# Kernel optimization log

Hardware: AMD Instinct MI355X
Metric: run time of the kernel (lower is better)

The kernel has to match this reference:

```python
import jax, jax.numpy as jnp
import numpy as np

B_SZ, SEQ, H, P, N, LBLK = 16, 2048, 16, 64, 16, 64  # batch, seqlen, heads, d_head, d_state, block_len


def setup_inputs() -> dict:
    key = jax.random.key(0)
    k1, k2, k3, k4 = jax.random.split(key, 4)
    X = jax.random.normal(k1, (B_SZ, SEQ, H, P), jnp.float32)
    # A is a per-step log-decay; real Mamba2 has A < 0 so exp(segsum) stays bounded
    A = -0.1 * jax.random.uniform(k2, (B_SZ, SEQ, H), jnp.float32)
    B = jax.random.normal(k3, (B_SZ, SEQ, H, N), jnp.float32)
    C = jax.random.normal(k4, (B_SZ, SEQ, H, N), jnp.float32)
    return {"X": X, "A": A, "B": B, "C": C}


def _exp_segsum(x):
    """x: (..., t). Returns exp(cumsum[i]-cumsum[j]) for j<=i, 0 above diagonal."""
    t = x.shape[-1]
    cs = jnp.cumsum(x, axis=-1)
    diff = cs[..., :, None] - cs[..., None, :]
    mask = jnp.tril(jnp.ones((t, t), dtype=bool))
    return jnp.where(mask, jnp.exp(jnp.where(mask, diff, 0.0)), 0.0)


def ssd_forward(X, A, B, C):
    b, s, h, p = X.shape
    n = B.shape[-1]
    c = s // LBLK
    # chunk: (b, c, l, h, *)
    Xb = X.reshape(b, c, LBLK, h, p)
    Bb = B.reshape(b, c, LBLK, h, n)
    Cb = C.reshape(b, c, LBLK, h, n)
    Ab = jnp.transpose(A.reshape(b, c, LBLK, h), (0, 3, 1, 2))  # (b, h, c, l)
    A_cs = jnp.cumsum(Ab, axis=-1)                               # (b, h, c, l)

    # 1. intra-chunk (diagonal block) output: kernel 1
    L = _exp_segsum(Ab)                                          # (b, h, c, l, s)
    CB = jnp.einsum("bclhn,bcshn->bhcls", Cb, Bb)               # (b, h, c, l, s)
    Y_diag = jnp.einsum("bhcls,bcshp->bclhp", CB * L, Xb)

    # 2. per-chunk end states: kernel 2
    decay_states = jnp.exp(A_cs[..., -1:] - A_cs)                # (b, h, c, l)
    states = jnp.einsum("bclhn,bhcl,bclhp->bchpn", Bb, decay_states, Xb)

    # 3. inter-chunk recurrence (zero initial state): kernel 3
    states = jnp.concatenate([jnp.zeros_like(states[:, :1]), states], axis=1)  # (b, c+1, h, p, n)
    A_last_pad = jnp.pad(A_cs[..., -1], ((0, 0), (0, 0), (1, 0)))              # (b, h, c+1)
    decay_chunk = _exp_segsum(A_last_pad)                                       # (b, h, c+1, c+1)
    new_states = jnp.einsum("bhzc,bchpn->bzhpn", decay_chunk, states)
    states_in = new_states[:, :-1]                                              # (b, c, h, p, n)

    # 4. off-diagonal (state -> output) contribution: kernel 4
    Y_off = jnp.einsum("bclhn,bchpn,bhcl->bclhp", Cb, states_in, jnp.exp(A_cs))

    return (Y_diag + Y_off).reshape(b, s, h, p)


def reference(X, A, B, C):
    return ssd_forward(X, A, B, C)
```

## Files before the change

kernel.cpp:

```cpp
#include <hip/hip_runtime.h>

#define BS 16
#define SEQL 2048
#define NH 16
#define PD 64
#define ND 16
#define LB 64
#define NC 32
#define NHP (NH * PD)
#define NHN (NH * ND)

typedef __attribute__((ext_vector_type(8))) short bf16x8;
typedef __attribute__((ext_vector_type(4))) float f32x4;

static __device__ __forceinline__ unsigned short f2bf(float x) {
  unsigned int u = __float_as_uint(x);
  return (unsigned short)((u + 0x7FFFu + ((u >> 16) & 1u)) >> 16);
}
static __device__ __forceinline__ unsigned int pk2(float a, float b) {
  return (unsigned int)f2bf(a) | ((unsigned int)f2bf(b) << 16);
}

static __device__ __forceinline__ void barrier_lds() {
  __builtin_amdgcn_sched_barrier(0);
  asm volatile("s_waitcnt lgkmcnt(0)" ::: "memory");
  __builtin_amdgcn_s_barrier();
  __builtin_amdgcn_sched_barrier(0);
}

static __device__ __forceinline__ int invperm(int l) {
  const int jp = l >> 5, v = l & 31;
  return jp * 32 + (v < 16 ? (((v >> 2) << 3) | (v & 3))
                           : ((((v - 16) >> 2) << 3) | 4 | ((v - 16) & 3)));
}

__global__ __launch_bounds__(512) void ssd_fused(
    const float* __restrict__ Xg, const float* __restrict__ Ag,
    const float* __restrict__ Bg, const float* __restrict__ Cg,
    float* __restrict__ Yg) {
  const int h = blockIdx.x & (NH - 1);
  const int b = blockIdx.x >> 4;
  const int t = threadIdx.x;
  const int w = t >> 6;
  const int lane = t & 63;
  const int g = lane >> 4;
  const int cc = lane & 15;

  __shared__ __align__(16) unsigned short sXt[2][PD][64];
  __shared__ __align__(16) unsigned short sB[2][LB][ND + 8];
  __shared__ __align__(16) unsigned short sC[2][LB][ND + 8];
  __shared__ __align__(16) unsigned short sBdT[2][ND][LB + 8];
  __shared__ __align__(16) float sSTf[2][PD][ND + 4];
  __shared__ __align__(16) unsigned short sSTb[2][PD][ND + 8];
  __shared__ float sER[NC][LB];
  __shared__ float sRR[NC][LB];
  __shared__ float sEtot[NC];

  {
    float av[4];
#pragma unroll
    for (int k = 0; k < 4; ++k)
      av[k] = Ag[((size_t)(b * SEQL + (w + 8 * k) * LB + lane)) * NH + h];
#pragma unroll
    for (int k = 0; k < 4; ++k) {
      const int c = w + 8 * k;
      float v = av[k];
#pragma unroll
      for (int d = 1; d < 64; d <<= 1) {
        float o = __shfl_up(v, d, 64);
        if (lane >= d) v += o;
      }
      const float e = expf(v);
      sER[c][lane] = e;
      sRR[c][lane] = expf(-v);
      if (lane == 63) sEtot[c] = e;
    }
  }
  for (int i = t; i < PD * (ND + 4); i += 512) ((float*)sSTf[0])[i] = 0.f;
  for (int i = t; i < PD * (ND + 8); i += 512) ((unsigned short*)sSTb[0])[i] = 0;

  const int xl0 = (t >> 4) * 2, xp0 = (t & 15) * 4;
  const int bl = t >> 3, bn0 = (t & 7) * 2;
  const int mX = invperm(xl0);
  const int mB = invperm(bl);
  float4 px0, px1;
  float2 pb2, pc2;

#define PREF(ci) do { \
    const size_t s0_ = (size_t)(b * SEQL + (ci) * LB); \
    px0 = *(const float4*)&Xg[(s0_ + xl0) * NHP + h * PD + xp0]; \
    px1 = *(const float4*)&Xg[(s0_ + xl0 + 1) * NHP + h * PD + xp0]; \
    pb2 = *(const float2*)&Bg[(s0_ + bl) * NHN + h * ND + bn0]; \
    pc2 = *(const float2*)&Cg[(s0_ + bl) * NHN + h * ND + bn0]; \
  } while (0)

#define STAGE(bufi, ci) do { \
    _Pragma("unroll") \
    for (int j_ = 0; j_ < 4; ++j_) { \
      const int p_ = xp0 + j_; \
      const int mm_ = ((((mX >> 3) ^ ((p_ >> 3) & 7)) << 3) | (mX & 7)); \
      *(unsigned int*)&sXt[bufi][p_][mm_] = pk2((&px0.x)[j_], (&px1.x)[j_]); \
    } \
    { const float el_ = sER[ci][bl]; \
      const float dl_ = sEtot[ci] * sRR[ci][bl]; \
      *(unsigned int*)&sB[bufi][bl][bn0] = pk2(pb2.x, pb2.y); \
      *(unsigned int*)&sC[bufi][bl][bn0] = pk2(el_ * pc2.x, el_ * pc2.y); \
      sBdT[bufi][bn0][mB] = f2bf(dl_ * pb2.x); \
      sBdT[bufi][bn0 + 1][mB] = f2bf(dl_ * pb2.y); } \
  } while (0)

  const bf16x8 zf8 = {0, 0, 0, 0, 0, 0, 0, 0};
  auto xfrag = [&](int buf, int p_, int kb) -> bf16x8 {
    return *(const bf16x8*)&sXt[buf][p_][(kb ^ ((p_ >> 3) & 7)) << 3];
  };

  PREF(0);
  STAGE(0, 0);
  PREF(1);
  barrier_lds();

  const int lb = w >> 1;
  const int pb0 = (w & 1) * 2;
  const int l = lb * 16 + cc;

  for (int c = 0; c < NC; ++c) {
    const int db = c & 1, nb = db ^ 1;

    bf16x8 cf = zf8;
    if (g < 2) cf = *(const bf16x8*)&sC[db][l][g * 8];
    auto mtile = [&](int sb, bool mask) -> uint2 {
      bf16x8 bfr = zf8;
      if (g < 2) bfr = *(const bf16x8*)&sB[db][sb * 16 + cc][g * 8];
      f32x4 z4 = {0.f, 0.f, 0.f, 0.f};
      f32x4 d = __builtin_amdgcn_mfma_f32_16x16x32_bf16(bfr, cf, z4, 0, 0, 0);
      float m[4];
#pragma unroll
      for (int r = 0; r < 4; ++r) {
        m[r] = d[r] * sRR[c][sb * 16 + 4 * g + r];
        if (mask && (4 * g + r) > cc) m[r] = 0.f;
      }
      return make_uint2(pk2(m[0], m[1]), pk2(m[2], m[3]));
    };
    union { bf16x8 v; unsigned int u[4]; } mf0, mf1;
    mf0.u[0] = mf0.u[1] = mf0.u[2] = mf0.u[3] = 0u;
    mf1.u[0] = mf1.u[1] = mf1.u[2] = mf1.u[3] = 0u;
    if (lb == 0) {
      const uint2 t0 = mtile(0, true);
      mf0.u[0] = t0.x; mf0.u[1] = t0.y;
    } else if (lb == 1) {
      const uint2 t0 = mtile(0, false), t1 = mtile(1, true);
      mf0.u[0] = t0.x; mf0.u[1] = t0.y; mf0.u[2] = t1.x; mf0.u[3] = t1.y;
    } else if (lb == 2) {
      const uint2 t0 = mtile(0, false), t1 = mtile(1, false), t2 = mtile(2, true);
      mf0.u[0] = t0.x; mf0.u[1] = t0.y; mf0.u[2] = t1.x; mf0.u[3] = t1.y;
      mf1.u[0] = t2.x; mf1.u[1] = t2.y;
    } else {
      const uint2 t0 = mtile(0, false), t1 = mtile(1, false);
      const uint2 t2 = mtile(2, false), t3 = mtile(3, true);
      mf0.u[0] = t0.x; mf0.u[1] = t0.y; mf0.u[2] = t1.x; mf0.u[3] = t1.y;
      mf1.u[0] = t2.x; mf1.u[1] = t2.y; mf1.u[2] = t3.x; mf1.u[3] = t3.y;
    }

#pragma unroll
    for (int pbi = 0; pbi < 2; ++pbi) {
      const int p = (pb0 + pbi) * 16 + cc;
      bf16x8 stf = zf8;
      if (g < 2) stf = *(const bf16x8*)&sSTb[db][p][g * 8];
      f32x4 acc = {0.f, 0.f, 0.f, 0.f};
      acc = __builtin_amdgcn_mfma_f32_16x16x32_bf16(cf, stf, acc, 0, 0, 0);
      acc = __builtin_amdgcn_mfma_f32_16x16x32_bf16(mf0.v, xfrag(db, p, g), acc, 0, 0, 0);
      if (lb >= 2)
        acc = __builtin_amdgcn_mfma_f32_16x16x32_bf16(mf1.v, xfrag(db, p, 4 + g), acc, 0, 0, 0);
      const size_t yb =
          ((size_t)(b * SEQL + c * LB + lb * 16 + 4 * g)) * NHP + h * PD + p;
#pragma unroll
      for (int r = 0; r < 4; ++r) Yg[yb + (size_t)r * NHP] = acc[r];
    }

    if (w < 4) {
      const int pS = w * 16 + cc;
      bf16x8 ad0 = *(const bf16x8*)&sBdT[db][cc][g * 8];
      bf16x8 ad1 = *(const bf16x8*)&sBdT[db][cc][32 + g * 8];
      f32x4 s4 = {0.f, 0.f, 0.f, 0.f};
      s4 = __builtin_amdgcn_mfma_f32_16x16x32_bf16(ad0, xfrag(db, pS, g), s4, 0, 0, 0);
      s4 = __builtin_amdgcn_mfma_f32_16x16x32_bf16(ad1, xfrag(db, pS, 4 + g), s4, 0, 0, 0);
      const float etot = sEtot[c];
      float4 old = *(const float4*)&sSTf[db][pS][4 * g];
      float4 nw;
      nw.x = old.x * etot + s4[0];
      nw.y = old.y * etot + s4[1];
      nw.z = old.z * etot + s4[2];
      nw.w = old.w * etot + s4[3];
      *(float4*)&sSTf[nb][pS][4 * g] = nw;
      uint2 ub;
      ub.x = pk2(nw.x, nw.y);
      ub.y = pk2(nw.z, nw.w);
      *(uint2*)&sSTb[nb][pS][4 * g] = ub;
    }

    if (c + 1 < NC) {
      STAGE(nb, c + 1);
      if (c + 2 < NC) PREF(c + 2);
    }
    barrier_lds();
  }
#undef PREF
#undef STAGE
}

extern "C" void kernel_launch(void* const* d_in, const int* in_sizes, int n_in,
                              void* d_out, int out_size, void* d_ws, size_t ws_size,
                              hipStream_t stream) {
  (void)in_sizes; (void)n_in; (void)out_size; (void)d_ws; (void)ws_size;
  const float* X = (const float*)d_in[0];
  const float* A = (const float*)d_in[1];
  const float* B = (const float*)d_in[2];
  const float* C = (const float*)d_in[3];
  float* Y = (float*)d_out;
  ssd_fused<<<BS * NH, 512, 0, stream>>>(X, A, B, C, Y);
}
```

Measured before the change: 75.57 us.

## Split head dimension across two blocks to double grid parallelism

Splits each (batch, head) block into two blocks that each own half of the P dimension, launching 512 blocks of 256 threads instead of 256 blocks of 512. This is meant to fill more CUs on the device and allow two blocks per CU. The cost is that B, C, A cumsum and the intra-chunk CB matrix are now computed redundantly in both halves. The transposed B staging is also rewritten to use coalesced per-thread loads.

```diff
diff --git a/kernel.cpp b/kernel.cpp
--- a/kernel.cpp
+++ b/kernel.cpp
@@ -9,6 +9,7 @@
 #define NC 32
 #define NHP (NH * PD)
 #define NHN (NH * ND)
+#define PH 32
 
 typedef __attribute__((ext_vector_type(8))) short bf16x8;
 typedef __attribute__((ext_vector_type(4))) float f32x4;
@@ -34,36 +35,39 @@
                            : ((((v - 16) >> 2) << 3) | 4 | ((v - 16) & 3)));
 }
 
-__global__ __launch_bounds__(512) void ssd_fused(
+__global__ __launch_bounds__(256, 2) void ssd_fused(
     const float* __restrict__ Xg, const float* __restrict__ Ag,
     const float* __restrict__ Bg, const float* __restrict__ Cg,
     float* __restrict__ Yg) {
-  const int h = blockIdx.x & (NH - 1);
-  const int b = blockIdx.x >> 4;
+  const int bh = blockIdx.x & 255;
+  const int phalf = blockIdx.x >> 8;
+  const int h = bh & (NH - 1);
+  const int b = bh >> 4;
+  const int pc0 = h * PD + phalf * PH;
   const int t = threadIdx.x;
   const int w = t >> 6;
   const int lane = t & 63;
   const int g = lane >> 4;
   const int cc = lane & 15;
 
-  __shared__ __align__(16) unsigned short sXt[2][PD][64];
+  __shared__ __align__(16) unsigned short sXt[2][PH][64];
   __shared__ __align__(16) unsigned short sB[2][LB][ND + 8];
   __shared__ __align__(16) unsigned short sC[2][LB][ND + 8];
   __shared__ __align__(16) unsigned short sBdT[2][ND][LB + 8];
-  __shared__ __align__(16) float sSTf[2][PD][ND + 4];
-  __shared__ __align__(16) unsigned short sSTb[2][PD][ND + 8];
+  __shared__ __align__(16) float sSTf[2][PH][ND + 4];
+  __shared__ __align__(16) unsigned short sSTb[2][PH][ND + 8];
   __shared__ float sER[NC][LB];
   __shared__ float sRR[NC][LB];
   __shared__ float sEtot[NC];
 
   {
-    float av[4];
-#pragma unroll
-    for (int k = 0; k < 4; ++k)
-      av[k] = Ag[((size_t)(b * SEQL + (w + 8 * k) * LB + lane)) * NH + h];
-#pragma unroll
-    for (int k = 0; k < 4; ++k) {
-      const int c = w + 8 * k;
+    float av[8];
+#pragma unroll
+    for (int k = 0; k < 8; ++k)
+      av[k] = Ag[((size_t)(b * SEQL + (w * 8 + k) * LB + lane)) * NH + h];
+#pragma unroll
+    for (int k = 0; k < 8; ++k) {
+      const int c = w * 8 + k;
       float v = av[k];
 #pragma unroll
       for (int d = 1; d < 64; d <<= 1) {
@@ -76,22 +80,31 @@
       if (lane == 63) sEtot[c] = e;
     }
   }
-  for (int i = t; i < PD * (ND + 4); i += 512) ((float*)sSTf[0])[i] = 0.f;
-  for (int i = t; i < PD * (ND + 8); i += 512) ((unsigned short*)sSTb[0])[i] = 0;
-
-  const int xl0 = (t >> 4) * 2, xp0 = (t & 15) * 4;
-  const int bl = t >> 3, bn0 = (t & 7) * 2;
+  for (int i = t; i < PH * (ND + 4); i += 256) ((float*)sSTf[0])[i] = 0.f;
+  for (int i = t; i < PH * (ND + 8); i += 256) ((unsigned short*)sSTb[0])[i] = 0;
+  __syncthreads();
+
+  const int xl0 = (t >> 3) * 2, xp0 = (t & 7) * 4;
+  const int bl = t >> 2, bn0 = (t & 3) * 4;
+  const int btn = t >> 4, btl = (t & 15) * 4;
   const int mX = invperm(xl0);
-  const int mB = invperm(bl);
-  float4 px0, px1;
-  float2 pb2, pc2;
+  int mb[4];
+#pragma unroll
+  for (int j = 0; j < 4; ++j) mb[j] = invperm(btl + j);
+
+  float4 px0, px1, pb4, pc4;
+  float pt0, pt1, pt2, pt3;
 
 #define PREF(ci) do { \
     const size_t s0_ = (size_t)(b * SEQL + (ci) * LB); \
-    px0 = *(const float4*)&Xg[(s0_ + xl0) * NHP + h * PD + xp0]; \
-    px1 = *(const float4*)&Xg[(s0_ + xl0 + 1) * NHP + h * PD + xp0]; \
-    pb2 = *(const float2*)&Bg[(s0_ + bl) * NHN + h * ND + bn0]; \
-    pc2 = *(const float2*)&Cg[(s0_ + bl) * NHN + h * ND + bn0]; \
+    px0 = *(const float4*)&Xg[(s0_ + xl0) * NHP + pc0 + xp0]; \
+    px1 = *(const float4*)&Xg[(s0_ + xl0 + 1) * NHP + pc0 + xp0]; \
+    pb4 = *(const float4*)&Bg[(s0_ + bl) * NHN + h * ND + bn0]; \
+    pc4 = *(const float4*)&Cg[(s0_ + bl) * NHN + h * ND + bn0]; \
+    pt0 = Bg[(s0_ + btl) * NHN + h * ND + btn]; \
+    pt1 = Bg[(s0_ + btl + 1) * NHN + h * ND + btn]; \
+    pt2 = Bg[(s0_ + btl + 2) * NHN + h * ND + btn]; \
+    pt3 = Bg[(s0_ + btl + 3) * NHN + h * ND + btn]; \
   } while (0)
 
 #define STAGE(bufi, ci) do { \
@@ -102,11 +115,17 @@
       *(unsigned int*)&sXt[bufi][p_][mm_] = pk2((&px0.x)[j_], (&px1.x)[j_]); \
     } \
     { const float el_ = sER[ci][bl]; \
-      const float dl_ = sEtot[ci] * sRR[ci][bl]; \
-      *(unsigned int*)&sB[bufi][bl][bn0] = pk2(pb2.x, pb2.y); \
-      *(unsigned int*)&sC[bufi][bl][bn0] = pk2(el_ * pc2.x, el_ * pc2.y); \
-      sBdT[bufi][bn0][mB] = f2bf(dl_ * pb2.x); \
-      sBdT[bufi][bn0 + 1][mB] = f2bf(dl_ * pb2.y); } \
+      uint2 ub_, uc_; \
+      ub_.x = pk2(pb4.x, pb4.y); ub_.y = pk2(pb4.z, pb4.w); \
+      uc_.x = pk2(el_ * pc4.x, el_ * pc4.y); \
+      uc_.y = pk2(el_ * pc4.z, el_ * pc4.w); \
+      *(uint2*)&sB[bufi][bl][bn0] = ub_; \
+      *(uint2*)&sC[bufi][bl][bn0] = uc_; } \
+    { const float et_ = sEtot[ci]; \
+      sBdT[bufi][btn][mb[0]] = f2bf(et_ * sRR[ci][btl] * pt0); \
+      sBdT[bufi][btn][mb[1]] = f2bf(et_ * sRR[ci][btl + 1] * pt1); \
+      sBdT[bufi][btn][mb[2]] = f2bf(et_ * sRR[ci][btl + 2] * pt2); \
+      sBdT[bufi][btn][mb[3]] = f2bf(et_ * sRR[ci][btl + 3] * pt3); } \
   } while (0)
 
   const bf16x8 zf8 = {0, 0, 0, 0, 0, 0, 0, 0};
@@ -119,9 +138,7 @@
   PREF(1);
   barrier_lds();
 
-  const int lb = w >> 1;
-  const int pb0 = (w & 1) * 2;
-  const int l = lb * 16 + cc;
+  const int l = w * 16 + cc;
 
   for (int c = 0; c < NC; ++c) {
     const int db = c & 1, nb = db ^ 1;
@@ -144,13 +161,13 @@
     union { bf16x8 v; unsigned int u[4]; } mf0, mf1;
     mf0.u[0] = mf0.u[1] = mf0.u[2] = mf0.u[3] = 0u;
     mf1.u[0] = mf1.u[1] = mf1.u[2] = mf1.u[3] = 0u;
-    if (lb == 0) {
+    if (w == 0) {
       const uint2 t0 = mtile(0, true);
       mf0.u[0] = t0.x; mf0.u[1] = t0.y;
-    } else if (lb == 1) {
+    } else if (w == 1) {
       const uint2 t0 = mtile(0, false), t1 = mtile(1, true);
       mf0.u[0] = t0.x; mf0.u[1] = t0.y; mf0.u[2] = t1.x; mf0.u[3] = t1.y;
-    } else if (lb == 2) {
+    } else if (w == 2) {
       const uint2 t0 = mtile(0, false), t1 = mtile(1, false), t2 = mtile(2, true);
       mf0.u[0] = t0.x; mf0.u[1] = t0.y; mf0.u[2] = t1.x; mf0.u[3] = t1.y;
       mf1.u[0] = t2.x; mf1.u[1] = t2.y;
@@ -163,21 +180,21 @@
 
 #pragma unroll
     for (int pbi = 0; pbi < 2; ++pbi) {
-      const int p = (pb0 + pbi) * 16 + cc;
+      const int p = pbi * 16 + cc;
       bf16x8 stf = zf8;
       if (g < 2) stf = *(const bf16x8*)&sSTb[db][p][g * 8];
       f32x4 acc = {0.f, 0.f, 0.f, 0.f};
       acc = __builtin_amdgcn_mfma_f32_16x16x32_bf16(cf, stf, acc, 0, 0, 0);
       acc = __builtin_amdgcn_mfma_f32_16x16x32_bf16(mf0.v, xfrag(db, p, g), acc, 0, 0, 0);
-      if (lb >= 2)
+      if (w >= 2)
         acc = __builtin_amdgcn_mfma_f32_16x16x32_bf16(mf1.v, xfrag(db, p, 4 + g), acc, 0, 0, 0);
       const size_t yb =
-          ((size_t)(b * SEQL + c * LB + lb * 16 + 4 * g)) * NHP + h * PD + p;
+          ((size_t)(b * SEQL + c * LB + w * 16 + 4 * g)) * NHP + pc0 + p;
 #pragma unroll
       for (int r = 0; r < 4; ++r) Yg[yb + (size_t)r * NHP] = acc[r];
     }
 
-    if (w < 4) {
+    if (w < 2) {
       const int pS = w * 16 + cc;
       bf16x8 ad0 = *(const bf16x8*)&sBdT[db][cc][g * 8];
       bf16x8 ad1 = *(const bf16x8*)&sBdT[db][cc][32 + g * 8];
@@ -217,5 +234,5 @@
   const float* B = (const float*)d_in[2];
   const float* C = (const float*)d_in[3];
   float* Y = (float*)d_out;
-  ssd_fused<<<BS * NH, 512, 0, stream>>>(X, A, B, C, Y);
-}
+  ssd_fused<<<2 * BS * NH, 256, 0, stream>>>(X, A, B, C, Y);
+}
```

Result: slower. 109.6 us (+45.0%).

## Process two chunks per barrier and keep per-wave state in registers

Applied to the files above, without the earlier changes.

Staging buffers grow from two to four slots so two chunks are staged and computed per barrier, halving barrier count. The inter-chunk state recurrence moves out of a shared fp32 buffer into per-wave registers, with each wave updating the state tile for its own p-columns and writing a private bf16 copy to LDS. The wave-to-(l,p) mapping and the B-transpose staging pattern change to match. This trades more registers, more LDS and redundant state MFMAs across waves for fewer synchronisations and no shared-state round trips.

```diff
diff --git a/kernel.cpp b/kernel.cpp
--- a/kernel.cpp
+++ b/kernel.cpp
@@ -46,12 +46,11 @@
   const int g = lane >> 4;
   const int cc = lane & 15;
 
-  __shared__ __align__(16) unsigned short sXt[2][PD][64];
-  __shared__ __align__(16) unsigned short sB[2][LB][ND + 8];
-  __shared__ __align__(16) unsigned short sC[2][LB][ND + 8];
-  __shared__ __align__(16) unsigned short sBdT[2][ND][LB + 8];
-  __shared__ __align__(16) float sSTf[2][PD][ND + 4];
-  __shared__ __align__(16) unsigned short sSTb[2][PD][ND + 8];
+  __shared__ __align__(16) unsigned short sXt[4][PD][64];
+  __shared__ __align__(16) unsigned short sB[4][LB][ND + 8];
+  __shared__ __align__(16) unsigned short sC[4][LB][ND + 8];
+  __shared__ __align__(16) unsigned short sBdT[4][ND][LB + 8];
+  __shared__ __align__(16) unsigned short sSTp[8][2][16][24];
   __shared__ float sER[NC][LB];
   __shared__ float sRR[NC][LB];
   __shared__ float sEtot[NC];
@@ -76,61 +75,83 @@
       if (lane == 63) sEtot[c] = e;
     }
   }
-  for (int i = t; i < PD * (ND + 4); i += 512) ((float*)sSTf[0])[i] = 0.f;
-  for (int i = t; i < PD * (ND + 8); i += 512) ((unsigned short*)sSTb[0])[i] = 0;
+  for (int i = t; i < 8 * 2 * 16 * 24; i += 512) ((unsigned short*)sSTp)[i] = 0;
 
   const int xl0 = (t >> 4) * 2, xp0 = (t & 15) * 4;
   const int bl = t >> 3, bn0 = (t & 7) * 2;
+  const int n_bt = t >> 5, l_bt = (t & 31) * 2;
   const int mX = invperm(xl0);
-  const int mB = invperm(bl);
-  float4 px0, px1;
-  float2 pb2, pc2;
-
-#define PREF(ci) do { \
+  const int mB = invperm(l_bt);
+  const int mB1 = invperm(l_bt + 1);
+
+  float4 px0A, px1A, px0B, px1B;
+  float2 pb2A, pc2A, pb2B, pc2B;
+  float pbAA, pbBA, pbAB, pbBB;
+
+#define PREFA(ci) do { \
     const size_t s0_ = (size_t)(b * SEQL + (ci) * LB); \
-    px0 = *(const float4*)&Xg[(s0_ + xl0) * NHP + h * PD + xp0]; \
-    px1 = *(const float4*)&Xg[(s0_ + xl0 + 1) * NHP + h * PD + xp0]; \
-    pb2 = *(const float2*)&Bg[(s0_ + bl) * NHN + h * ND + bn0]; \
-    pc2 = *(const float2*)&Cg[(s0_ + bl) * NHN + h * ND + bn0]; \
+    px0A = *(const float4*)&Xg[(s0_ + xl0) * NHP + h * PD + xp0]; \
+    px1A = *(const float4*)&Xg[(s0_ + xl0 + 1) * NHP + h * PD + xp0]; \
+    pb2A = *(const float2*)&Bg[(s0_ + bl) * NHN + h * ND + bn0]; \
+    pc2A = *(const float2*)&Cg[(s0_ + bl) * NHN + h * ND + bn0]; \
+    pbAA = Bg[(s0_ + l_bt) * NHN + h * ND + n_bt]; \
+    pbBA = Bg[(s0_ + l_bt + 1) * NHN + h * ND + n_bt]; \
   } while (0)
-
-#define STAGE(bufi, ci) do { \
+#define PREFB(ci) do { \
+    const size_t s0_ = (size_t)(b * SEQL + (ci) * LB); \
+    px0B = *(const float4*)&Xg[(s0_ + xl0) * NHP + h * PD + xp0]; \
+    px1B = *(const float4*)&Xg[(s0_ + xl0 + 1) * NHP + h * PD + xp0]; \
+    pb2B = *(const float2*)&Bg[(s0_ + bl) * NHN + h * ND + bn0]; \
+    pc2B = *(const float2*)&Cg[(s0_ + bl) * NHN + h * ND + bn0]; \
+    pbAB = Bg[(s0_ + l_bt) * NHN + h * ND + n_bt]; \
+    pbBB = Bg[(s0_ + l_bt + 1) * NHN + h * ND + n_bt]; \
+  } while (0)
+
+#define STAGE(px0_, px1_, pb2_, pc2_, pbA_, pbB_, slot, ci) do { \
     _Pragma("unroll") \
     for (int j_ = 0; j_ < 4; ++j_) { \
       const int p_ = xp0 + j_; \
       const int mm_ = ((((mX >> 3) ^ ((p_ >> 3) & 7)) << 3) | (mX & 7)); \
-      *(unsigned int*)&sXt[bufi][p_][mm_] = pk2((&px0.x)[j_], (&px1.x)[j_]); \
+      *(unsigned int*)&sXt[slot][p_][mm_] = pk2((&px0_.x)[j_], (&px1_.x)[j_]); \
     } \
     { const float el_ = sER[ci][bl]; \
-      const float dl_ = sEtot[ci] * sRR[ci][bl]; \
-      *(unsigned int*)&sB[bufi][bl][bn0] = pk2(pb2.x, pb2.y); \
-      *(unsigned int*)&sC[bufi][bl][bn0] = pk2(el_ * pc2.x, el_ * pc2.y); \
-      sBdT[bufi][bn0][mB] = f2bf(dl_ * pb2.x); \
-      sBdT[bufi][bn0 + 1][mB] = f2bf(dl_ * pb2.y); } \
+      *(unsigned int*)&sB[slot][bl][bn0] = pk2(pb2_.x, pb2_.y); \
+      *(unsigned int*)&sC[slot][bl][bn0] = pk2(el_ * pc2_.x, el_ * pc2_.y); } \
+    { const float et_ = sEtot[ci]; \
+      sBdT[slot][n_bt][mB]  = f2bf(et_ * sRR[ci][l_bt] * pbA_); \
+      sBdT[slot][n_bt][mB1] = f2bf(et_ * sRR[ci][l_bt + 1] * pbB_); } \
   } while (0)
 
   const bf16x8 zf8 = {0, 0, 0, 0, 0, 0, 0, 0};
-  auto xfrag = [&](int buf, int p_, int kb) -> bf16x8 {
-    return *(const bf16x8*)&sXt[buf][p_][(kb ^ ((p_ >> 3) & 7)) << 3];
+  auto xfrag = [&](int slot, int p_, int kb) -> bf16x8 {
+    return *(const bf16x8*)&sXt[slot][p_][(kb ^ ((p_ >> 3) & 7)) << 3];
   };
 
-  PREF(0);
-  STAGE(0, 0);
-  PREF(1);
+  const int lb = w & 3;
+  const int pb0 = (w >> 2) * 2;
+  const int l = lb * 16 + cc;
+  float stm[2][4];
+#pragma unroll
+  for (int i = 0; i < 2; ++i)
+#pragma unroll
+    for (int r = 0; r < 4; ++r) stm[i][r] = 0.f;
+
+  __syncthreads();
+
+  PREFA(0);
+  PREFB(1);
+  STAGE(px0A, px1A, pb2A, pc2A, pbAA, pbBA, 0, 0);
+  STAGE(px0B, px1B, pb2B, pc2B, pbAB, pbBB, 1, 1);
+  PREFA(2);
+  PREFB(3);
   barrier_lds();
 
-  const int lb = w >> 1;
-  const int pb0 = (w & 1) * 2;
-  const int l = lb * 16 + cc;
-
-  for (int c = 0; c < NC; ++c) {
-    const int db = c & 1, nb = db ^ 1;
-
+  auto compute_chunk = [&](int slot, int c) {
     bf16x8 cf = zf8;
-    if (g < 2) cf = *(const bf16x8*)&sC[db][l][g * 8];
+    if (g < 2) cf = *(const bf16x8*)&sC[slot][l][g * 8];
     auto mtile = [&](int sb, bool mask) -> uint2 {
       bf16x8 bfr = zf8;
-      if (g < 2) bfr = *(const bf16x8*)&sB[db][sb * 16 + cc][g * 8];
+      if (g < 2) bfr = *(const bf16x8*)&sB[slot][sb * 16 + cc][g * 8];
       f32x4 z4 = {0.f, 0.f, 0.f, 0.f};
       f32x4 d = __builtin_amdgcn_mfma_f32_16x16x32_bf16(bfr, cf, z4, 0, 0, 0);
       float m[4];
@@ -160,51 +181,52 @@
       mf0.u[0] = t0.x; mf0.u[1] = t0.y; mf0.u[2] = t1.x; mf0.u[3] = t1.y;
       mf1.u[0] = t2.x; mf1.u[1] = t2.y; mf1.u[2] = t3.x; mf1.u[3] = t3.y;
     }
-
+    bf16x8 ad0 = *(const bf16x8*)&sBdT[slot][cc][g * 8];
+    bf16x8 ad1 = *(const bf16x8*)&sBdT[slot][cc][32 + g * 8];
+    const float etot = sEtot[c];
 #pragma unroll
     for (int pbi = 0; pbi < 2; ++pbi) {
       const int p = (pb0 + pbi) * 16 + cc;
       bf16x8 stf = zf8;
-      if (g < 2) stf = *(const bf16x8*)&sSTb[db][p][g * 8];
+      if (g < 2) stf = *(const bf16x8*)&sSTp[w][pbi][cc][g * 8];
       f32x4 acc = {0.f, 0.f, 0.f, 0.f};
       acc = __builtin_amdgcn_mfma_f32_16x16x32_bf16(cf, stf, acc, 0, 0, 0);
-      acc = __builtin_amdgcn_mfma_f32_16x16x32_bf16(mf0.v, xfrag(db, p, g), acc, 0, 0, 0);
+      acc = __builtin_amdgcn_mfma_f32_16x16x32_bf16(mf0.v, xfrag(slot, p, g), acc, 0, 0, 0);
       if (lb >= 2)
-        acc = __builtin_amdgcn_mfma_f32_16x16x32_bf16(mf1.v, xfrag(db, p, 4 + g), acc, 0, 0, 0);
+        acc = __builtin_amdgcn_mfma_f32_16x16x32_bf16(mf1.v, xfrag(slot, p, 4 + g), acc, 0, 0, 0);
       const size_t yb =
           ((size_t)(b * SEQL + c * LB + lb * 16 + 4 * g)) * NHP + h * PD + p;
 #pragma unroll
       for (int r = 0; r < 4; ++r) Yg[yb + (size_t)r * NHP] = acc[r];
-    }
-
-    if (w < 4) {
-      const int pS = w * 16 + cc;
-      bf16x8 ad0 = *(const bf16x8*)&sBdT[db][cc][g * 8];
-      bf16x8 ad1 = *(const bf16x8*)&sBdT[db][cc][32 + g * 8];
       f32x4 s4 = {0.f, 0.f, 0.f, 0.f};
-      s4 = __builtin_amdgcn_mfma_f32_16x16x32_bf16(ad0, xfrag(db, pS, g), s4, 0, 0, 0);
-      s4 = __builtin_amdgcn_mfma_f32_16x16x32_bf16(ad1, xfrag(db, pS, 4 + g), s4, 0, 0, 0);
-      const float etot = sEtot[c];
-      float4 old = *(const float4*)&sSTf[db][pS][4 * g];
-      float4 nw;
-      nw.x = old.x * etot + s4[0];
-      nw.y = old.y * etot + s4[1];
-      nw.z = old.z * etot + s4[2];
-      nw.w = old.w * etot + s4[3];
-      *(float4*)&sSTf[nb][pS][4 * g] = nw;
+      s4 = __builtin_amdgcn_mfma_f32_16x16x32_bf16(ad0, xfrag(slot, p, g), s4, 0, 0, 0);
+      s4 = __builtin_amdgcn_mfma_f32_16x16x32_bf16(ad1, xfrag(slot, p, 4 + g), s4, 0, 0, 0);
+#pragma unroll
+      for (int r = 0; r < 4; ++r) stm[pbi][r] = stm[pbi][r] * etot + s4[r];
       uint2 ub;
-      ub.x = pk2(nw.x, nw.y);
-      ub.y = pk2(nw.z, nw.w);
-      *(uint2*)&sSTb[nb][pS][4 * g] = ub;
-    }
-
-    if (c + 1 < NC) {
-      STAGE(nb, c + 1);
-      if (c + 2 < NC) PREF(c + 2);
+      ub.x = pk2(stm[pbi][0], stm[pbi][1]);
+      ub.y = pk2(stm[pbi][2], stm[pbi][3]);
+      *(uint2*)&sSTp[w][pbi][cc][4 * g] = ub;
+    }
+  };
+
+  for (int k = 0; k < 16; ++k) {
+    const int sA = (k & 1) * 2, sB_ = sA + 1;
+    compute_chunk(sA, 2 * k);
+    compute_chunk(sB_, 2 * k + 1);
+    if (k < 15) {
+      const int dA = (~k & 1) * 2, dB = dA + 1;
+      STAGE(px0A, px1A, pb2A, pc2A, pbAA, pbBA, dA, 2 * k + 2);
+      STAGE(px0B, px1B, pb2B, pc2B, pbAB, pbBB, dB, 2 * k + 3);
+      if (k < 14) {
+        PREFA(2 * k + 4);
+        PREFB(2 * k + 5);
+      }
     }
     barrier_lds();
   }
-#undef PREF
+#undef PREFA
+#undef PREFB
 #undef STAGE
 }
 
```

Result: slower. 105.3 us (+39.4%).
